# Kernel optimization log

Hardware: AMD Instinct MI355X
Metric: run time of the kernel (lower is better)

## Reference

```python
import jax, jax.numpy as jnp
import numpy as np

DIM = 512; NHEAD = 8; DHEAD = 64; INNER = NHEAD * DHEAD
CTX = 1024; NOCT = int(np.ceil(np.log2(CTX))) + 1  # 11
B = 8; SEQ = 256; MEM = 768


def positional_encoding(ctx, num_oct):
    # matches Attention.positional_encoding on coords=arange(ctx).view(ctx,1),
    # start_octave = 1 - num_oct
    coords = jnp.arange(ctx, dtype=jnp.float32)[:, None, None]        # (ctx,1,1)
    octaves = jnp.arange(1 - num_oct, 1, dtype=jnp.float32)           # (num_oct,)
    mult = (2.0 ** octaves) * np.pi
    scaled = (coords * mult).reshape(ctx, num_oct)                    # (ctx, num_oct)
    return jnp.concatenate([jnp.sin(scaled), jnp.cos(scaled)], axis=-1)  # (ctx, 2*num_oct)


def get_shifts(mem, seq, ctx):
    coords = jnp.arange(mem + seq - 1, -1, -1) - (seq - 1)            # (mem+seq,)
    shifts = coords[None, :] + jnp.arange(seq)[:, None]               # (seq, mem+seq)
    oob = (shifts < 0) | (shifts > ctx - 1)
    bias = jnp.where(oob, -jnp.inf, 0.0).astype(jnp.float32)
    return jnp.clip(shifts, 0, ctx - 1), bias


def setup_inputs() -> dict:
    key = jax.random.key(0)
    ks = jax.random.split(key, 8)
    s = 0.02
    return {
        "x": jax.random.normal(ks[0], (B, SEQ, DIM), jnp.float32),
        "memory": jax.random.normal(ks[1], (B, MEM, DIM), jnp.float32),
        "W_qkv": jax.random.normal(ks[2], (DIM, 3 * INNER), jnp.float32) * s,
        "W_rel": jax.random.normal(ks[3], (2 * NOCT, INNER), jnp.float32) * s,
        "W_out": jax.random.normal(ks[4], (INNER, DIM), jnp.float32) * s,
        "b_out": jnp.zeros((DIM,), jnp.float32),
        "u_emb": jax.random.normal(ks[5], (DHEAD,), jnp.float32),
        "v_emb": jax.random.normal(ks[6], (DHEAD,), jnp.float32),
    }


def reference(x, memory, W_qkv, W_rel, W_out, b_out, u_emb, v_emb):
    b, seq, _ = x.shape
    mem = memory.shape[1]
    total = mem + seq
    scale = DHEAD ** -0.5

    shifts, bias = get_shifts(mem, seq, CTX)                          # (seq,total) each
    R = positional_encoding(CTX, NOCT)                                # (CTX, 2*NOCT)
    kr = (R @ W_rel)[shifts].reshape(seq, total, NHEAD, DHEAD)        # n m h d

    qkv = jnp.concatenate([memory, x], axis=1) @ W_qkv                # (b,total,3*INNER)
    q, k, v = jnp.split(qkv, 3, axis=-1)

    def heads(t):
        return t.reshape(b, total, NHEAD, DHEAD).transpose(0, 2, 1, 3)  # b h m d

    q = heads(q)[:, :, mem:]                                          # b h n d (queries only over x)
    k = heads(k)
    v = heads(v)

    term_a = jnp.einsum('bhnd,bhmd->bhnm', q, k)
    term_b = jnp.einsum('bhnd,nmhd->bhnm', q, kr)
    term_c = jnp.einsum('d,bhmd->bhm', u_emb, k)[:, :, None, :]        # broadcast over n
    term_d = jnp.einsum('d,nmhd->hnm', v_emb, kr)[None]                # broadcast over b

    dots = (term_a + term_b + term_c + term_d) * scale + bias          # banded -inf mask
    attn = jax.nn.softmax(dots, axis=-1)                               # dropout p=0 -> identity
    out = jnp.einsum('bhnm,bhmd->bnhd', attn, v).reshape(b, seq, INNER)
    return out @ W_out + b_out
```

## Files before the change

### kernel.cpp

```cpp
#include <hip/hip_runtime.h>
#include <hip/hip_bf16.h>
#include <math.h>

typedef unsigned short u16;
typedef unsigned int u32;
typedef __attribute__((ext_vector_type(8))) short short8;
typedef __attribute__((ext_vector_type(4))) float floatx4;

constexpr int kB     = 8;
constexpr int kSEQ   = 256;
constexpr int kMEM   = 768;
constexpr int kTOTAL = 1024;

__device__ __forceinline__ float bf2f(u16 u) {
  return __uint_as_float(((u32)u) << 16);
}
__device__ __forceinline__ u16 f2bf(float f) {
  __hip_bfloat16 h = __float2bfloat16(f);
  return *reinterpret_cast<u16*>(&h);
}
__device__ __forceinline__ void gload_lds16(const u16* g, u16* l) {
  __builtin_amdgcn_global_load_lds(
      (__attribute__((address_space(1))) const unsigned int*)g,
      (__attribute__((address_space(3))) unsigned int*)l, 16, 0, 0);
}

__device__ __forceinline__ void wtconv_body(
    const float* __restrict__ W, u16* __restrict__ Wt, int K, int N,
    int n0, int k0, int tid, float (*tile)[65])
{
  int r = tid >> 4, c4 = (tid & 15) * 4;
#pragma unroll
  for (int v = 0; v < 4; v++) {
    float4 w4 = *(const float4*)(W + (size_t)(k0 + v * 16 + r) * N + n0 + c4);
    tile[v * 16 + r][c4 + 0] = w4.x;
    tile[v * 16 + r][c4 + 1] = w4.y;
    tile[v * 16 + r][c4 + 2] = w4.z;
    tile[v * 16 + r][c4 + 3] = w4.w;
  }
  __syncthreads();
#pragma unroll
  for (int v = 0; v < 4; v++) {
    int rn = v * 16 + r;
    ushort4 o;
    o.x = f2bf(tile[c4 + 0][rn]);
    o.y = f2bf(tile[c4 + 1][rn]);
    o.z = f2bf(tile[c4 + 2][rn]);
    o.w = f2bf(tile[c4 + 3][rn]);
    *(ushort4*)(Wt + (size_t)(n0 + rn) * K + k0 + c4) = o;
  }
}

__global__ __launch_bounds__(256) void prep_kernel(
    const float* __restrict__ x, const float* __restrict__ memf,
    const float* __restrict__ W_qkv, const float* __restrict__ W_out,
    const float* __restrict__ W_rel, const float* __restrict__ v_emb,
    const float* __restrict__ u_emb,
    u16* __restrict__ Xb, u16* __restrict__ WqkvT, u16* __restrict__ WoutT,
    u16* __restrict__ Rrel_bf, float* __restrict__ vR)
{
  __shared__ float tile[64][65];
  __shared__ float pe[22];
  __shared__ float prod[512];
  int bid = blockIdx.x;
  int t = threadIdx.x;
  if (bid < 1024) {
    int s = bid;
    if (t < 22) {
      int o = (t < 11) ? t : (t - 11);
      float mult = ldexpf(3.14159265358979323846f, o - 10);
      float ang = (float)s * mult;
      pe[t] = (t < 11) ? sinf(ang) : cosf(ang);
    }
    __syncthreads();
#pragma unroll
    for (int c = 0; c < 2; c++) {
      int j = t + c * 256;
      float acc = 0.f;
#pragma unroll
      for (int o = 0; o < 22; ++o) acc += pe[o] * W_rel[o * 512 + j];
      u16 rbf = f2bf(acc);
      Rrel_bf[(size_t)s * 512 + j] = rbf;
      prod[j] = acc * v_emb[j & 63] - bf2f(rbf) * u_emb[j & 63];
    }
    __syncthreads();
    if (t < 8) {
      float a = 0.f;
#pragma unroll 8
      for (int d = 0; d < 64; d++) a += prod[t * 64 + d];
      vR[t * 1024 + s] = a * 0.125f;
    }
  } else if (bid < 3072) {
    int idx = (bid - 1024) * 256 + t;
    int row = idx >> 6, c8 = idx & 63;
    int b = row >> 10, pos = row & 1023;
    const float* src = (pos < kMEM)
        ? memf + (size_t)(b * kMEM + pos) * 512
        : x    + (size_t)(b * kSEQ + pos - kMEM) * 512;
    const float4* s4 = (const float4*)(src + c8 * 8);
    float4 a = s4[0], bb = s4[1];
    u16 tmp[8] = {f2bf(a.x),  f2bf(a.y),  f2bf(a.z),  f2bf(a.w),
                  f2bf(bb.x), f2bf(bb.y), f2bf(bb.z), f2bf(bb.w)};
    *(uint4*)(Xb + (size_t)row * 512 + c8 * 8) = *(uint4*)tmp;
  } else if (bid < 3264) {
    int r = bid - 3072;
    wtconv_body(W_qkv, WqkvT, 512, 1536, (r % 24) * 64, (r / 24) * 64, t, tile);
  } else {
    int r = bid - 3264;
    wtconv_body(W_out, WoutT, 512, 512, (r % 8) * 64, (r / 8) * 64, t, tile);
  }
}

__global__ __launch_bounds__(256) void gemm_bf16(
    const u16* __restrict__ A, const u16* __restrict__ Bt,
    int lda, int ldb, int ksteps,
    u16* __restrict__ Cbf, int ldc, int qscale, const float* __restrict__ uq)
{
  __shared__ u16 As[128 * 64];
  __shared__ u16 Bs[128 * 64];
  int tid = threadIdx.x;
  int id = blockIdx.y * gridDim.x + blockIdx.x;
  int gy = gridDim.y;
  int bm = (id % gy) * 128, bn = (id / gy) * 128;
  if (qscale && bn < 512 && ((bm >> 7) & 7) < 6) return;
  int ln = tid & 15, quad = (tid >> 4) & 3, w = tid >> 6;
  int moff = (w >> 1) * 64, noff = (w & 1) * 64;
  int l7 = ln & 7;
  floatx4 acc[4][4];
#pragma unroll
  for (int mi = 0; mi < 4; mi++)
#pragma unroll
    for (int ni = 0; ni < 4; ni++) acc[mi][ni] = (floatx4){0.f, 0.f, 0.f, 0.f};

  int srow[4], sgch[4];
#pragma unroll
  for (int v = 0; v < 4; v++) {
    int f = v * 256 + tid;
    srow[v] = f >> 3;
    sgch[v] = (f & 7) ^ ((f >> 3) & 7);
  }

  for (int ks = 0; ks < ksteps; ks++) {
    int k0 = ks * 64;
#pragma unroll
    for (int v = 0; v < 4; v++) {
      gload_lds16(A + (size_t)(bm + srow[v]) * lda + k0 + sgch[v] * 8,
                  &As[(v * 256 + tid) * 8]);
      gload_lds16(Bt + (size_t)(bn + srow[v]) * ldb + k0 + sgch[v] * 8,
                  &Bs[(v * 256 + tid) * 8]);
    }
    __syncthreads();
#pragma unroll
    for (int kb = 0; kb < 2; kb++) {
      short8 af[4], bfr[4];
#pragma unroll
      for (int mi = 0; mi < 4; mi++) {
        int row = moff + mi * 16 + ln;
        af[mi] = *(const short8*)&As[row * 64 + (((quad + 4 * kb) ^ l7) << 3)];
      }
#pragma unroll
      for (int ni = 0; ni < 4; ni++) {
        int row = noff + ni * 16 + ln;
        bfr[ni] = *(const short8*)&Bs[row * 64 + (((quad + 4 * kb) ^ l7) << 3)];
      }
#pragma unroll
      for (int mi = 0; mi < 4; mi++)
#pragma unroll
        for (int ni = 0; ni < 4; ni++)
          acc[mi][ni] = __builtin_amdgcn_mfma_f32_16x16x32_bf16(
              af[mi], bfr[ni], acc[mi][ni], 0, 0, 0);
    }
    __syncthreads();
  }

  int r0 = bm + moff + quad * 4;
#pragma unroll
  for (int ni = 0; ni < 4; ni++) {
    int col = bn + noff + ni * 16 + ln;
    bool isq = qscale && col < 512;
    float scale = isq ? 0.125f : 1.f;
    float uadd = isq ? uq[col & 63] : 0.f;
#pragma unroll
    for (int mi = 0; mi < 4; mi++) {
#pragma unroll
      for (int r = 0; r < 4; r++) {
        int row = r0 + mi * 16 + r;
        Cbf[(size_t)row * ldc + col] = f2bf((acc[mi][ni][r] + uadd) * scale);
      }
    }
  }
}

__global__ __launch_bounds__(256) void gemm_bf16_64(
    const u16* __restrict__ A, const u16* __restrict__ Bt,
    int lda, int ldb, int ksteps,
    float* __restrict__ Cf, int ldc, const float* __restrict__ bias)
{
  __shared__ u16 As[64 * 64];
  __shared__ u16 Bs[64 * 64];
  int tid = threadIdx.x;
  int id = blockIdx.y * gridDim.x + blockIdx.x;
  int gy = gridDim.y;
  int bm = (id % gy) * 64, bn = (id / gy) * 64;
  int ln = tid & 15, quad = (tid >> 4) & 3, w = tid >> 6;
  int moff = (w >> 1) * 32, noff = (w & 1) * 32;
  int l7 = ln & 7;
  floatx4 acc[2][2];
#pragma unroll
  for (int mi = 0; mi < 2; mi++)
#pragma unroll
    for (int ni = 0; ni < 2; ni++) acc[mi][ni] = (floatx4){0.f, 0.f, 0.f, 0.f};

  int srow[2], sgch[2];
#pragma unroll
  for (int v = 0; v < 2; v++) {
    int f = v * 256 + tid;
    srow[v] = f >> 3;
    sgch[v] = (f & 7) ^ ((f >> 3) & 7);
  }

  for (int ks = 0; ks < ksteps; ks++) {
    int k0 = ks * 64;
#pragma unroll
    for (int v = 0; v < 2; v++) {
      gload_lds16(A + (size_t)(bm + srow[v]) * lda + k0 + sgch[v] * 8,
                  &As[(v * 256 + tid) * 8]);
      gload_lds16(Bt + (size_t)(bn + srow[v]) * ldb + k0 + sgch[v] * 8,
                  &Bs[(v * 256 + tid) * 8]);
    }
    __syncthreads();
#pragma unroll
    for (int kb = 0; kb < 2; kb++) {
      short8 af[2], bfr[2];
#pragma unroll
      for (int mi = 0; mi < 2; mi++) {
        int row = moff + mi * 16 + ln;
        af[mi] = *(const short8*)&As[row * 64 + (((quad + 4 * kb) ^ l7) << 3)];
      }
#pragma unroll
      for (int ni = 0; ni < 2; ni++) {
        int row = noff + ni * 16 + ln;
        bfr[ni] = *(const short8*)&Bs[row * 64 + (((quad + 4 * kb) ^ l7) << 3)];
      }
#pragma unroll
      for (int mi = 0; mi < 2; mi++)
#pragma unroll
        for (int ni = 0; ni < 2; ni++)
          acc[mi][ni] = __builtin_amdgcn_mfma_f32_16x16x32_bf16(
              af[mi], bfr[ni], acc[mi][ni], 0, 0, 0);
    }
    __syncthreads();
  }

  int r0 = bm + moff + quad * 4;
#pragma unroll
  for (int ni = 0; ni < 2; ni++) {
    int col = bn + noff + ni * 16 + ln;
    float cv = bias[col];
#pragma unroll
    for (int mi = 0; mi < 2; mi++) {
#pragma unroll
      for (int r = 0; r < 4; r++) {
        int row = r0 + mi * 16 + r;
        Cf[(size_t)row * ldc + col] = acc[mi][ni][r] + cv;
      }
    }
  }
}

__global__ __launch_bounds__(256) void attn_mfma(
    const u16* __restrict__ qkv_bf, const u16* __restrict__ Rrel_bf,
    const float* __restrict__ vR,
    u16* __restrict__ Opart, float* __restrict__ lbuf)
{
  constexpr int LD = 72;
  __shared__ u16 Vt[2][64 * LD];
  __shared__ u16 Ps[64 * LD];

  int h = blockIdx.x;
  int nt = blockIdx.y >> 2, p = blockIdx.y & 3;
  int b = blockIdx.z;
  int n0 = nt * 64, bh = b * 8 + h;
  int tid = threadIdx.x;
  int w = tid >> 6, lane = tid & 63;
  int l15 = lane & 15, quad = lane >> 4, q8 = quad * 8;

  int sr0 = tid >> 3, sc8 = tid & 7;
  int sr1 = (256 + tid) >> 3;
  int vg0 = ((sr0 >> 3) ^ sc8) * 8 + (sr0 & 7);
  int vg1 = ((sr1 >> 3) ^ sc8) * 8 + (sr1 & 7);

  const u16* kpart = qkv_bf + (size_t)(b * kTOTAL) * 1536 + 512 + h * 64;
  const float* vRh = vR + h * 1024;
  int s_base_w = kMEM + n0 + 16 * w;

  const u16* qrow = qkv_bf + (size_t)(b * kTOTAL + kMEM + n0 + 16 * w + l15) * 1536 + h * 64;
  short8 qf0 = *(const short8*)(qrow + q8);
  short8 qf1 = *(const short8*)(qrow + 32 + q8);

  int bidx[4];
#pragma unroll
  for (int r = 0; r < 4; r++) {
    int il = 4 * quad + r;
    bidx[r] = ((quad << 4) | ((il + 15 - l15) & 15)) << 2;
  }

  auto load_V = [&](int mtu, int mtv, uint4 (&vr)[4]) {
    const u16* va = kpart + (size_t)mtu * 64 * 1536 + 512;
    const u16* vb = kpart + (size_t)mtv * 64 * 1536 + 512;
    vr[0] = *(const uint4*)(va + (size_t)sr0 * 1536 + sc8 * 8);
    vr[1] = *(const uint4*)(va + (size_t)sr1 * 1536 + sc8 * 8);
    vr[2] = *(const uint4*)(vb + (size_t)sr0 * 1536 + sc8 * 8);
    vr[3] = *(const uint4*)(vb + (size_t)sr1 * 1536 + sc8 * 8);
  };
  auto write_V = [&](uint4 (&vr)[4], u16* bu, u16* bv) {
    const u16* c0 = (const u16*)&vr[0];
    const u16* c1 = (const u16*)&vr[1];
    const u16* c2 = (const u16*)&vr[2];
    const u16* c3 = (const u16*)&vr[3];
#pragma unroll
    for (int i = 0; i < 8; i++) {
      bu[(sc8 * 8 + i) * LD + vg0] = c0[i];
      bu[(sc8 * 8 + i) * LD + vg1] = c1[i];
      bv[(sc8 * 8 + i) * LD + vg0] = c2[i];
      bv[(sc8 * 8 + i) * LD + vg1] = c3[i];
    }
  };
  auto load_K = [&](int mt, short8 (&k0)[4], short8 (&k1)[4]) {
#pragma unroll
    for (int ni = 0; ni < 4; ni++) {
      const u16* kr = kpart + (size_t)(mt * 64 + 16 * ni + l15) * 1536;
      k0[ni] = *(const short8*)(kr + q8);
      k1[ni] = *(const short8*)(kr + 32 + q8);
    }
  };
  auto load_R = [&](int sb, short8 (&r0)[5], short8 (&r1)[5], float (&vc)[5]) {
#pragma unroll
    for (int ct = 0; ct < 5; ct++) {
      int s = sb - 63 + 16 * ct + l15;
      s = min(max(s, 0), 1023);
      const u16* rr = Rrel_bf + (size_t)s * 512 + h * 64;
      r0[ct] = *(const short8*)(rr + q8);
      r1[ct] = *(const short8*)(rr + 32 + q8);
      vc[ct] = vRh[s];
    }
  };

  floatx4 o_acc[4];
  float l_i[4];
#pragma unroll
  for (int r = 0; r < 4; r++) l_i[r] = 0.f;
#pragma unroll
  for (int nd = 0; nd < 4; nd++) o_acc[nd] = (floatx4){0.f, 0.f, 0.f, 0.f};

  auto do_T = [&](short8 (&rb0)[5], short8 (&rb1)[5], float (&vRc)[5],
                  float (&tf)[5][4]) {
#pragma unroll
    for (int ct = 0; ct < 5; ct++) {
      floatx4 t = (floatx4){0.f, 0.f, 0.f, 0.f};
      t = __builtin_amdgcn_mfma_f32_16x16x32_bf16(qf0, rb0[ct], t, 0, 0, 0);
      t = __builtin_amdgcn_mfma_f32_16x16x32_bf16(qf1, rb1[ct], t, 0, 0, 0);
#pragma unroll
      for (int r = 0; r < 4; r++) tf[ct][r] = t[r] + vRc[ct];
    }
  };
  auto do_tsh = [&](float (&tf)[5][4], float (&tsh)[4][4]) {
#pragma unroll
    for (int ni = 0; ni < 4; ni++) {
#pragma unroll
      for (int r = 0; r < 4; r++) {
        int il = 4 * quad + r;
        float tv = (l15 < il) ? tf[4 - ni][r] : tf[3 - ni][r];
        tsh[ni][r] = __int_as_float(
            __builtin_amdgcn_ds_bpermute(bidx[r], __float_as_int(tv)));
      }
    }
  };
  auto do_QK = [&](short8 (&kb0)[4], short8 (&kb1)[4], floatx4 (&sa)[4]) {
#pragma unroll
    for (int ni = 0; ni < 4; ni++) {
      floatx4 s4 = (floatx4){0.f, 0.f, 0.f, 0.f};
      s4 = __builtin_amdgcn_mfma_f32_16x16x32_bf16(qf0, kb0[ni], s4, 0, 0, 0);
      s4 = __builtin_amdgcn_mfma_f32_16x16x32_bf16(qf1, kb1[ni], s4, 0, 0, 0);
      sa[ni] = s4;
    }
  };
  auto do_logits = [&](floatx4 (&sa)[4], float (&tsh)[4][4], int sb) {
#pragma unroll
    for (int ni = 0; ni < 4; ni++) {
#pragma unroll
      for (int r = 0; r < 4; r++) {
        int il = 4 * quad + r;
        float val = sa[ni][r] + tsh[ni][r];
        if ((16 * ni + l15) > (sb + il)) val = -1e30f;
        float e = __expf(val);
        l_i[r] += e;
        int prow = 16 * w + il;
        Ps[prow * LD + (l15 & 7) + (((2 * ni + (l15 >> 3)) ^ (prow >> 3)) << 3)] =
            f2bf(e);
      }
    }
  };
  auto do_PV = [&](const u16* VtX) {
    int rowq = 16 * w + l15, rr3q = rowq >> 3;
    short8 pa0 = *(const short8*)&Ps[rowq * LD + ((quad ^ rr3q) << 3)];
    short8 pa1 = *(const short8*)&Ps[rowq * LD + (((quad + 4) ^ rr3q) << 3)];
#pragma unroll
    for (int nd = 0; nd < 4; nd++) {
      int rowv = 16 * nd + l15, rr3v = rowv >> 3;
      short8 vb0 = *(const short8*)&VtX[rowv * LD + ((quad ^ rr3v) << 3)];
      short8 vb1 = *(const short8*)&VtX[rowv * LD + (((quad + 4) ^ rr3v) << 3)];
      o_acc[nd] = __builtin_amdgcn_mfma_f32_16x16x32_bf16(pa0, vb0, o_acc[nd], 0, 0, 0);
      o_acc[nd] = __builtin_amdgcn_mfma_f32_16x16x32_bf16(pa1, vb1, o_acc[nd], 0, 0, 0);
    }
  };

  short8 rbU0[5], rbU1[5];
  float vRcU[5];
  uint4 vsl[4];
  {
    uint4 v0[4];
    load_V(p, p + 4, v0);
    write_V(v0, Vt[0], Vt[1]);
  }
  load_V(p + 8, p + 12, vsl);
  load_R(s_base_w - 64 * p, rbU0, rbU1, vRcU);
  __syncthreads();

#pragma unroll
  for (int g = 0; g < 2; g++) {
    int mtU = p + 8 * g, mtV = mtU + 4;
    int sbU = s_base_w - 64 * mtU, sbV = s_base_w - 64 * mtV;

    if (g == 1) write_V(vsl, Vt[0], Vt[1]);

    short8 kbU0[4], kbU1[4];
    load_K(mtU, kbU0, kbU1);

    float tfU[5][4], tshU[4][4];
    do_T(rbU0, rbU1, vRcU, tfU);
    do_tsh(tfU, tshU);

    short8 rbV0[5], rbV1[5];
    float vRcV[5];
    load_R(sbV, rbV0, rbV1, vRcV);

    floatx4 saU[4];
    do_QK(kbU0, kbU1, saU);
    do_logits(saU, tshU, sbU);

    short8 kbV0[4], kbV1[4];
    load_K(mtV, kbV0, kbV1);
    if (g == 0)
      load_R(s_base_w - 64 * (p + 8), rbU0, rbU1, vRcU);

    float tfV[5][4], tshV[4][4];
    do_T(rbV0, rbV1, vRcV, tfV);
    do_tsh(tfV, tshV);

    if (g == 1) __syncthreads();
    do_PV(Vt[0]);

    floatx4 saV[4];
    do_QK(kbV0, kbV1, saV);
    do_logits(saV, tshV, sbV);
    do_PV(Vt[1]);

    if (g == 0) __syncthreads();
  }

  int pbase = (p * 64 + bh) * 256;
#pragma unroll
  for (int r = 0; r < 4; r++) {
    float l = l_i[r];
#pragma unroll
    for (int off = 1; off < 16; off <<= 1)
      l += __shfl_xor(l, off, 64);
    int n = n0 + 16 * w + 4 * quad + r;
    u16* orow = Opart + ((size_t)(pbase + n) << 6) + l15;
#pragma unroll
    for (int nd = 0; nd < 4; nd++)
      orow[16 * nd] = f2bf(o_acc[nd][r]);
    if (l15 == 0) lbuf[pbase + n] = l;
  }
}

__global__ __launch_bounds__(256) void attn_combine(
    const u16* __restrict__ Opart, const float* __restrict__ lbuf,
    u16* __restrict__ aout_bf)
{
  int idx = blockIdx.x * 256 + threadIdx.x;
  int bh = idx >> 12, n = (idx >> 4) & 255, d4 = idx & 15;
  int rowi = bh * 256 + n;
  float den = 0.f;
  float num[4] = {0.f, 0.f, 0.f, 0.f};
#pragma unroll
  for (int p = 0; p < 4; p++) {
    den += lbuf[(p << 14) + rowi];
    uint2 raw = *(const uint2*)(Opart + (((size_t)(p << 14) + rowi) << 6) + d4 * 4);
    const u16* us = (const u16*)&raw;
#pragma unroll
    for (int j = 0; j < 4; j++) num[j] += bf2f(us[j]);
  }
  float inv = 1.f / den;
  int b = bh >> 3, h = bh & 7;
  ushort4 o;
  o.x = f2bf(num[0] * inv);
  o.y = f2bf(num[1] * inv);
  o.z = f2bf(num[2] * inv);
  o.w = f2bf(num[3] * inv);
  *(ushort4*)(aout_bf + (size_t)(b * kSEQ + n) * 512 + h * 64 + d4 * 4) = o;
}

extern "C" void kernel_launch(void* const* d_in, const int* in_sizes, int n_in,
                              void* d_out, int out_size, void* d_ws, size_t ws_size,
                              hipStream_t stream) {
  (void)in_sizes; (void)n_in; (void)out_size; (void)ws_size;
  const float* x      = (const float*)d_in[0];
  const float* memory = (const float*)d_in[1];
  const float* W_qkv  = (const float*)d_in[2];
  const float* W_rel  = (const float*)d_in[3];
  const float* W_out  = (const float*)d_in[4];
  const float* b_out  = (const float*)d_in[5];
  const float* u_emb  = (const float*)d_in[6];
  const float* v_emb  = (const float*)d_in[7];
  float* out = (float*)d_out;

  char* ws = (char*)d_ws;
  u16*   qkv_bf  = (u16*)ws;                         ws += (size_t)12582912 * 2;
  u16*   Xcat_bf = (u16*)ws;                         ws += (size_t)4194304 * 2;
  u16*   aout_bf = (u16*)ws;                         ws += (size_t)1048576 * 2;
  u16*   Opart   = (u16*)ws;                         ws += (size_t)4194304 * 2;
  float* lbuf    = (float*)ws;                       ws += (size_t)65536 * 4;
  u16*   WqkvT   = (u16*)ws;                         ws += (size_t)786432 * 2;
  u16*   WoutT   = (u16*)ws;                         ws += (size_t)262144 * 2;
  u16*   Rrel_bf = (u16*)ws;                         ws += (size_t)524288 * 2;
  float* vR      = (float*)ws;                       ws += (size_t)8192 * 4;

  prep_kernel<<<3328, 256, 0, stream>>>(
      x, memory, W_qkv, W_out, W_rel, v_emb, u_emb,
      Xcat_bf, WqkvT, WoutT, Rrel_bf, vR);

  gemm_bf16<<<dim3(12, 64), 256, 0, stream>>>(
      Xcat_bf, WqkvT, 512, 512, 8, qkv_bf, 1536, 1, u_emb);

  attn_mfma<<<dim3(8, 16, 8), 256, 0, stream>>>(
      qkv_bf, Rrel_bf, vR, Opart, lbuf);

  attn_combine<<<1024, 256, 0, stream>>>(Opart, lbuf, aout_bf);

  gemm_bf16_64<<<dim3(8, 32), 256, 0, stream>>>(
      aout_bf, WoutT, 512, 512, 8, out, 512, b_out);
}
```

Baseline: 150.3 us.

## Fuse attention partial combine into output GEMM, shrink QKV tiles, add MFMA priority

The separate attn_combine kernel and its aout_bf buffer are removed. The output projection GEMM now reads the four partial Opart slices plus lbuf, normalises them, and writes the A tile into LDS itself. This saves one launch and an intermediate round trip through global memory, at the cost of redundant partial reads across the 8 column blocks. The QKV GEMM moves to 64x128 tiles for more blocks and better occupancy, and s_setprio is raised around MFMA sections in the attention kernel.

```diff
diff --git a/kernel.cpp b/kernel.cpp
--- a/kernel.cpp
+++ b/kernel.cpp
@@ -111,24 +111,22 @@
   }
 }
 
-__global__ __launch_bounds__(256) void gemm_bf16(
+__global__ __launch_bounds__(256) void gemm_qkv(
     const u16* __restrict__ A, const u16* __restrict__ Bt,
-    int lda, int ldb, int ksteps,
-    u16* __restrict__ Cbf, int ldc, int qscale, const float* __restrict__ uq)
+    u16* __restrict__ Cbf, const float* __restrict__ uq)
 {
-  __shared__ u16 As[128 * 64];
+  __shared__ u16 As[64 * 64];
   __shared__ u16 Bs[128 * 64];
   int tid = threadIdx.x;
   int id = blockIdx.y * gridDim.x + blockIdx.x;
-  int gy = gridDim.y;
-  int bm = (id % gy) * 128, bn = (id / gy) * 128;
-  if (qscale && bn < 512 && ((bm >> 7) & 7) < 6) return;
+  int bm = (id % 128) * 64, bn = (id / 128) * 128;
+  if (bn < 512 && ((bm >> 6) & 15) < 12) return;
   int ln = tid & 15, quad = (tid >> 4) & 3, w = tid >> 6;
-  int moff = (w >> 1) * 64, noff = (w & 1) * 64;
+  int moff = (w >> 1) * 32, noff = (w & 1) * 64;
   int l7 = ln & 7;
-  floatx4 acc[4][4];
-#pragma unroll
-  for (int mi = 0; mi < 4; mi++)
+  floatx4 acc[2][4];
+#pragma unroll
+  for (int mi = 0; mi < 2; mi++)
 #pragma unroll
     for (int ni = 0; ni < 4; ni++) acc[mi][ni] = (floatx4){0.f, 0.f, 0.f, 0.f};
 
@@ -140,21 +138,22 @@
     sgch[v] = (f & 7) ^ ((f >> 3) & 7);
   }
 
-  for (int ks = 0; ks < ksteps; ks++) {
+  for (int ks = 0; ks < 8; ks++) {
     int k0 = ks * 64;
 #pragma unroll
-    for (int v = 0; v < 4; v++) {
-      gload_lds16(A + (size_t)(bm + srow[v]) * lda + k0 + sgch[v] * 8,
+    for (int v = 0; v < 2; v++)
+      gload_lds16(A + (size_t)(bm + srow[v]) * 512 + k0 + sgch[v] * 8,
                   &As[(v * 256 + tid) * 8]);
-      gload_lds16(Bt + (size_t)(bn + srow[v]) * ldb + k0 + sgch[v] * 8,
+#pragma unroll
+    for (int v = 0; v < 4; v++)
+      gload_lds16(Bt + (size_t)(bn + srow[v]) * 512 + k0 + sgch[v] * 8,
                   &Bs[(v * 256 + tid) * 8]);
-    }
     __syncthreads();
 #pragma unroll
     for (int kb = 0; kb < 2; kb++) {
-      short8 af[4], bfr[4];
-#pragma unroll
-      for (int mi = 0; mi < 4; mi++) {
+      short8 af[2], bfr[4];
+#pragma unroll
+      for (int mi = 0; mi < 2; mi++) {
         int row = moff + mi * 16 + ln;
         af[mi] = *(const short8*)&As[row * 64 + (((quad + 4 * kb) ^ l7) << 3)];
       }
@@ -164,7 +163,7 @@
         bfr[ni] = *(const short8*)&Bs[row * 64 + (((quad + 4 * kb) ^ l7) << 3)];
       }
 #pragma unroll
-      for (int mi = 0; mi < 4; mi++)
+      for (int mi = 0; mi < 2; mi++)
 #pragma unroll
         for (int ni = 0; ni < 4; ni++)
           acc[mi][ni] = __builtin_amdgcn_mfma_f32_16x16x32_bf16(
@@ -177,92 +176,15 @@
 #pragma unroll
   for (int ni = 0; ni < 4; ni++) {
     int col = bn + noff + ni * 16 + ln;
-    bool isq = qscale && col < 512;
+    bool isq = col < 512;
     float scale = isq ? 0.125f : 1.f;
     float uadd = isq ? uq[col & 63] : 0.f;
 #pragma unroll
-    for (int mi = 0; mi < 4; mi++) {
+    for (int mi = 0; mi < 2; mi++) {
 #pragma unroll
       for (int r = 0; r < 4; r++) {
         int row = r0 + mi * 16 + r;
-        Cbf[(size_t)row * ldc + col] = f2bf((acc[mi][ni][r] + uadd) * scale);
-      }
-    }
-  }
-}
-
-__global__ __launch_bounds__(256) void gemm_bf16_64(
-    const u16* __restrict__ A, const u16* __restrict__ Bt,
-    int lda, int ldb, int ksteps,
-    float* __restrict__ Cf, int ldc, const float* __restrict__ bias)
-{
-  __shared__ u16 As[64 * 64];
-  __shared__ u16 Bs[64 * 64];
-  int tid = threadIdx.x;
-  int id = blockIdx.y * gridDim.x + blockIdx.x;
-  int gy = gridDim.y;
-  int bm = (id % gy) * 64, bn = (id / gy) * 64;
-  int ln = tid & 15, quad = (tid >> 4) & 3, w = tid >> 6;
-  int moff = (w >> 1) * 32, noff = (w & 1) * 32;
-  int l7 = ln & 7;
-  floatx4 acc[2][2];
-#pragma unroll
-  for (int mi = 0; mi < 2; mi++)
-#pragma unroll
-    for (int ni = 0; ni < 2; ni++) acc[mi][ni] = (floatx4){0.f, 0.f, 0.f, 0.f};
-
-  int srow[2], sgch[2];
-#pragma unroll
-  for (int v = 0; v < 2; v++) {
-    int f = v * 256 + tid;
-    srow[v] = f >> 3;
-    sgch[v] = (f & 7) ^ ((f >> 3) & 7);
-  }
-
-  for (int ks = 0; ks < ksteps; ks++) {
-    int k0 = ks * 64;
-#pragma unroll
-    for (int v = 0; v < 2; v++) {
-      gload_lds16(A + (size_t)(bm + srow[v]) * lda + k0 + sgch[v] * 8,
-                  &As[(v * 256 + tid) * 8]);
-      gload_lds16(Bt + (size_t)(bn + srow[v]) * ldb + k0 + sgch[v] * 8,
-                  &Bs[(v * 256 + tid) * 8]);
-    }
-    __syncthreads();
-#pragma unroll
-    for (int kb = 0; kb < 2; kb++) {
-      short8 af[2], bfr[2];
-#pragma unroll
-      for (int mi = 0; mi < 2; mi++) {
-        int row = moff + mi * 16 + ln;
-        af[mi] = *(const short8*)&As[row * 64 + (((quad + 4 * kb) ^ l7) << 3)];
-      }
-#pragma unroll
-      for (int ni = 0; ni < 2; ni++) {
-        int row = noff + ni * 16 + ln;
-        bfr[ni] = *(const short8*)&Bs[row * 64 + (((quad + 4 * kb) ^ l7) << 3)];
-      }
-#pragma unroll
-      for (int mi = 0; mi < 2; mi++)
-#pragma unroll
-        for (int ni = 0; ni < 2; ni++)
-          acc[mi][ni] = __builtin_amdgcn_mfma_f32_16x16x32_bf16(
-              af[mi], bfr[ni], acc[mi][ni], 0, 0, 0);
-    }
-    __syncthreads();
-  }
-
-  int r0 = bm + moff + quad * 4;
-#pragma unroll
-  for (int ni = 0; ni < 2; ni++) {
-    int col = bn + noff + ni * 16 + ln;
-    float cv = bias[col];
-#pragma unroll
-    for (int mi = 0; mi < 2; mi++) {
-#pragma unroll
-      for (int r = 0; r < 4; r++) {
-        int row = r0 + mi * 16 + r;
-        Cf[(size_t)row * ldc + col] = acc[mi][ni][r] + cv;
+        Cbf[(size_t)row * 1536 + col] = f2bf((acc[mi][ni][r] + uadd) * scale);
       }
     }
   }
@@ -355,6 +277,7 @@
 
   auto do_T = [&](short8 (&rb0)[5], short8 (&rb1)[5], float (&vRc)[5],
                   float (&tf)[5][4]) {
+    __builtin_amdgcn_s_setprio(1);
 #pragma unroll
     for (int ct = 0; ct < 5; ct++) {
       floatx4 t = (floatx4){0.f, 0.f, 0.f, 0.f};
@@ -363,6 +286,7 @@
 #pragma unroll
       for (int r = 0; r < 4; r++) tf[ct][r] = t[r] + vRc[ct];
     }
+    __builtin_amdgcn_s_setprio(0);
   };
   auto do_tsh = [&](float (&tf)[5][4], float (&tsh)[4][4]) {
 #pragma unroll
@@ -377,6 +301,7 @@
     }
   };
   auto do_QK = [&](short8 (&kb0)[4], short8 (&kb1)[4], floatx4 (&sa)[4]) {
+    __builtin_amdgcn_s_setprio(1);
 #pragma unroll
     for (int ni = 0; ni < 4; ni++) {
       floatx4 s4 = (floatx4){0.f, 0.f, 0.f, 0.f};
@@ -384,6 +309,7 @@
       s4 = __builtin_amdgcn_mfma_f32_16x16x32_bf16(qf1, kb1[ni], s4, 0, 0, 0);
       sa[ni] = s4;
     }
+    __builtin_amdgcn_s_setprio(0);
   };
   auto do_logits = [&](floatx4 (&sa)[4], float (&tsh)[4][4], int sb) {
 #pragma unroll
@@ -405,6 +331,7 @@
     int rowq = 16 * w + l15, rr3q = rowq >> 3;
     short8 pa0 = *(const short8*)&Ps[rowq * LD + ((quad ^ rr3q) << 3)];
     short8 pa1 = *(const short8*)&Ps[rowq * LD + (((quad + 4) ^ rr3q) << 3)];
+    __builtin_amdgcn_s_setprio(1);
 #pragma unroll
     for (int nd = 0; nd < 4; nd++) {
       int rowv = 16 * nd + l15, rr3v = rowv >> 3;
@@ -413,6 +340,7 @@
       o_acc[nd] = __builtin_amdgcn_mfma_f32_16x16x32_bf16(pa0, vb0, o_acc[nd], 0, 0, 0);
       o_acc[nd] = __builtin_amdgcn_mfma_f32_16x16x32_bf16(pa1, vb1, o_acc[nd], 0, 0, 0);
     }
+    __builtin_amdgcn_s_setprio(0);
   };
 
   short8 rbU0[5], rbU1[5];
@@ -485,31 +413,123 @@
   }
 }
 
-__global__ __launch_bounds__(256) void attn_combine(
+__global__ __launch_bounds__(256) void gemm_out_fused(
     const u16* __restrict__ Opart, const float* __restrict__ lbuf,
-    u16* __restrict__ aout_bf)
+    const u16* __restrict__ Bt, float* __restrict__ Cf,
+    const float* __restrict__ bias)
 {
-  int idx = blockIdx.x * 256 + threadIdx.x;
-  int bh = idx >> 12, n = (idx >> 4) & 255, d4 = idx & 15;
-  int rowi = bh * 256 + n;
-  float den = 0.f;
-  float num[4] = {0.f, 0.f, 0.f, 0.f};
-#pragma unroll
-  for (int p = 0; p < 4; p++) {
-    den += lbuf[(p << 14) + rowi];
-    uint2 raw = *(const uint2*)(Opart + (((size_t)(p << 14) + rowi) << 6) + d4 * 4);
-    const u16* us = (const u16*)&raw;
-#pragma unroll
-    for (int j = 0; j < 4; j++) num[j] += bf2f(us[j]);
-  }
-  float inv = 1.f / den;
-  int b = bh >> 3, h = bh & 7;
-  ushort4 o;
-  o.x = f2bf(num[0] * inv);
-  o.y = f2bf(num[1] * inv);
-  o.z = f2bf(num[2] * inv);
-  o.w = f2bf(num[3] * inv);
-  *(ushort4*)(aout_bf + (size_t)(b * kSEQ + n) * 512 + h * 64 + d4 * 4) = o;
+  __shared__ u16 As[64 * 64];
+  __shared__ u16 Bs[64 * 64];
+  __shared__ float invl[64][8];
+  int tid = threadIdx.x;
+  int id = blockIdx.y * gridDim.x + blockIdx.x;
+  int bm = (id % 32) * 64, bn = (id / 32) * 64;
+  int ln = tid & 15, quad = (tid >> 4) & 3, w = tid >> 6;
+  int moff = (w >> 1) * 32, noff = (w & 1) * 32;
+  int l7 = ln & 7;
+
+#pragma unroll
+  for (int e = tid; e < 512; e += 256) {
+    int r = e >> 3, hh = e & 7;
+    int grow = bm + r, b = grow >> 8, n = grow & 255;
+    int bh = b * 8 + hh;
+    float den = 0.f;
+#pragma unroll
+    for (int p = 0; p < 4; p++) den += lbuf[((p * 64 + bh) << 8) + n];
+    invl[r][hh] = 1.f / den;
+  }
+
+  floatx4 acc[2][2];
+#pragma unroll
+  for (int mi = 0; mi < 2; mi++)
+#pragma unroll
+    for (int ni = 0; ni < 2; ni++) acc[mi][ni] = (floatx4){0.f, 0.f, 0.f, 0.f};
+
+  int srow[2], sgch[2];
+#pragma unroll
+  for (int v = 0; v < 2; v++) {
+    int f = v * 256 + tid;
+    srow[v] = f >> 3;
+    sgch[v] = (f & 7) ^ ((f >> 3) & 7);
+  }
+
+  int sr = tid >> 2, dq = (tid & 3) * 16;
+  int growq = bm + sr, bq = growq >> 8, nq = growq & 255;
+  int cg0 = dq >> 3;
+  u16* dst0 = &As[sr * 64 + ((cg0 ^ (sr & 7)) << 3)];
+  u16* dst1 = &As[sr * 64 + (((cg0 + 1) ^ (sr & 7)) << 3)];
+
+  __syncthreads();
+
+  for (int ks = 0; ks < 8; ks++) {
+    int k0 = ks * 64;
+#pragma unroll
+    for (int v = 0; v < 2; v++)
+      gload_lds16(Bt + (size_t)(bn + srow[v]) * 512 + k0 + sgch[v] * 8,
+                  &Bs[(v * 256 + tid) * 8]);
+
+    {
+      const u16* ob = Opart + (((size_t)(bq * 8 + ks) << 8) + nq) * 64 + dq;
+      float inv = invl[sr][ks];
+      float sum[16];
+#pragma unroll
+      for (int j = 0; j < 16; j++) sum[j] = 0.f;
+#pragma unroll
+      for (int p = 0; p < 4; p++) {
+        const u16* src = ob + ((size_t)p << 20);
+        uint4 r0 = *(const uint4*)src;
+        uint4 r1 = *(const uint4*)(src + 8);
+        const u16* u0 = (const u16*)&r0;
+        const u16* u1 = (const u16*)&r1;
+#pragma unroll
+        for (int j = 0; j < 8; j++) sum[j] += bf2f(u0[j]);
+#pragma unroll
+        for (int j = 0; j < 8; j++) sum[8 + j] += bf2f(u1[j]);
+      }
+      u16 ov[16];
+#pragma unroll
+      for (int j = 0; j < 16; j++) ov[j] = f2bf(sum[j] * inv);
+      *(uint4*)dst0 = *(uint4*)&ov[0];
+      *(uint4*)dst1 = *(uint4*)&ov[8];
+    }
+    __syncthreads();
+#pragma unroll
+    for (int kb = 0; kb < 2; kb++) {
+      short8 af[2], bfr[2];
+#pragma unroll
+      for (int mi = 0; mi < 2; mi++) {
+        int row = moff + mi * 16 + ln;
+        af[mi] = *(const short8*)&As[row * 64 + (((quad + 4 * kb) ^ l7) << 3)];
+      }
+#pragma unroll
+      for (int ni = 0; ni < 2; ni++) {
+        int row = noff + ni * 16 + ln;
+        bfr[ni] = *(const short8*)&Bs[row * 64 + (((quad + 4 * kb) ^ l7) << 3)];
+      }
+#pragma unroll
+      for (int mi = 0; mi < 2; mi++)
+#pragma unroll
+        for (int ni = 0; ni < 2; ni++)
+          acc[mi][ni] = __builtin_amdgcn_mfma_f32_16x16x32_bf16(
+              af[mi], bfr[ni], acc[mi][ni], 0, 0, 0);
+    }
+    __syncthreads();
+  }
+
+  int r0 = bm + moff + quad * 4;
+#pragma unroll
+  for (int ni = 0; ni < 2; ni++) {
+    int col = bn + noff + ni * 16 + ln;
+    float cv = bias[col];
+#pragma unroll
+    for (int mi = 0; mi < 2; mi++) {
+#pragma unroll
+      for (int r = 0; r < 4; r++) {
+        int row = r0 + mi * 16 + r;
+        Cf[(size_t)row * 512 + col] = acc[mi][ni][r] + cv;
+      }
+    }
+  }
 }
 
 extern "C" void kernel_launch(void* const* d_in, const int* in_sizes, int n_in,
@@ -529,7 +549,6 @@
   char* ws = (char*)d_ws;
   u16*   qkv_bf  = (u16*)ws;                         ws += (size_t)12582912 * 2;
   u16*   Xcat_bf = (u16*)ws;                         ws += (size_t)4194304 * 2;
-  u16*   aout_bf = (u16*)ws;                         ws += (size_t)1048576 * 2;
   u16*   Opart   = (u16*)ws;                         ws += (size_t)4194304 * 2;
   float* lbuf    = (float*)ws;                       ws += (size_t)65536 * 4;
   u16*   WqkvT   = (u16*)ws;                         ws += (size_t)786432 * 2;
@@ -541,14 +560,12 @@
       x, memory, W_qkv, W_out, W_rel, v_emb, u_emb,
       Xcat_bf, WqkvT, WoutT, Rrel_bf, vR);
 
-  gemm_bf16<<<dim3(12, 64), 256, 0, stream>>>(
-      Xcat_bf, WqkvT, 512, 512, 8, qkv_bf, 1536, 1, u_emb);
+  gemm_qkv<<<dim3(12, 128), 256, 0, stream>>>(
+      Xcat_bf, WqkvT, qkv_bf, u_emb);
 
   attn_mfma<<<dim3(8, 16, 8), 256, 0, stream>>>(
       qkv_bf, Rrel_bf, vR, Opart, lbuf);
 
-  attn_combine<<<1024, 256, 0, stream>>>(Opart, lbuf, aout_bf);
-
-  gemm_bf16_64<<<dim3(8, 32), 256, 0, stream>>>(
-      aout_bf, WoutT, 512, 512, 8, out, 512, b_out);
-}
+  gemm_out_fused<<<dim3(8, 32), 256, 0, stream>>>(
+      Opart, lbuf, WoutT, out, b_out);
+}
```

Result: slower. 157.4 us (+4.7%).
